# Kernel optimization log

Hardware: AMD Instinct MI355X
Metric: run time of the kernel (lower is better)

## Reference

```python
import jax, jax.numpy as jnp
import numpy as np

N_NODES = 100000
N_EDGES = 1600000
N_GRAPHS = 128
IN_DIM, HID, OUT_DIM, DOC_DIM = 64, 128, 32, 768
LAYERS = 3


def setup_inputs() -> dict:
    key = jax.random.key(0)
    ks = jax.random.split(key, 24)
    s = 0.05
    inp = {
        "x": jax.random.normal(ks[0], (N_NODES, IN_DIM), jnp.float32),
        "doc_features": jax.random.normal(ks[1], (N_GRAPHS, DOC_DIM), jnp.float32),
        "edge_index": jax.random.randint(ks[2], (2, N_EDGES), 0, N_NODES, jnp.int64),
        "batch": jnp.sort(jax.random.randint(ks[3], (N_NODES,), 0, N_GRAPHS, jnp.int64)),
        # parameters (stored as [in, out] so y = x @ W + b)
        "node_w": jax.random.normal(ks[4], (IN_DIM, HID), jnp.float32) * s,
        "node_b": jnp.zeros((HID,), jnp.float32),
        "ggnn_w": jax.random.normal(ks[5], (LAYERS, HID, HID), jnp.float32) * s,
        "gru_w_ih": jax.random.normal(ks[6], (HID, 3 * HID), jnp.float32) * s,
        "gru_b_ih": jnp.zeros((3 * HID,), jnp.float32),
        "gru_w_hh": jax.random.normal(ks[7], (HID, 3 * HID), jnp.float32) * s,
        "gru_b_hh": jnp.zeros((3 * HID,), jnp.float32),
        "doc_w": jax.random.normal(ks[8], (DOC_DIM, HID), jnp.float32) * s,
        "doc_b": jnp.zeros((HID,), jnp.float32),
        "ln_g": jnp.ones((2 * HID,), jnp.float32),
        "ln_b": jnp.zeros((2 * HID,), jnp.float32),
        "fus_w": jax.random.normal(ks[9], (2 * HID, HID), jnp.float32) * s,
        "fus_b": jnp.zeros((HID,), jnp.float32),
        "task_w": jax.random.normal(ks[10], (HID, OUT_DIM), jnp.float32) * s,
        "task_b": jnp.zeros((OUT_DIM,), jnp.float32),
        "time_w": jax.random.normal(ks[11], (HID, 1), jnp.float32) * s,
        "time_b": jnp.zeros((1,), jnp.float32),
    }
    return inp


def _gru(m, h, w_ih, b_ih, w_hh, b_hh):
    gi = m @ w_ih + b_ih  # [N, 3H]
    gh = h @ w_hh + b_hh
    ir, iz, in_ = jnp.split(gi, 3, axis=-1)
    hr, hz, hn = jnp.split(gh, 3, axis=-1)
    r = jax.nn.sigmoid(ir + hr)
    z = jax.nn.sigmoid(iz + hz)
    n = jnp.tanh(in_ + r * hn)
    return (1.0 - z) * n + z * h


def reference(x, doc_features, node_w, node_b, ggnn_w, gru_w_ih, gru_b_ih,
              gru_w_hh, gru_b_hh, doc_w, doc_b, ln_g, ln_b, fus_w, fus_b,
              task_w, task_b, time_w, time_b, edge_index, batch):
    N = x.shape[0]
    src, dst = edge_index[0], edge_index[1]
    # node projection + ReLU
    h = jax.nn.relu(x @ node_w + node_b)  # [N, H]
    # GatedGraphConv: 3 layers of (linear -> scatter-add over edges -> GRU)
    for i in range(LAYERS):
        m = h @ ggnn_w[i]                              # [N, H]
        agg = jax.ops.segment_sum(m[src], dst, num_segments=N)  # scatter-add
        h = _gru(agg, h, gru_w_ih, gru_b_ih, gru_w_hh, gru_b_hh)
    # global mean pool over graphs
    sums = jax.ops.segment_sum(h, batch, num_segments=N_GRAPHS)  # [G, H]
    cnt = jax.ops.segment_sum(jnp.ones((N,), h.dtype), batch, num_segments=N_GRAPHS)
    pooled = sums / jnp.maximum(cnt, 1.0)[:, None]
    # doc projection + fusion head
    doc_emb = jax.nn.relu(doc_features @ doc_w + doc_b)  # [G, H]
    fusion = jnp.concatenate([pooled, doc_emb], axis=1)  # [G, 2H]
    mu = jnp.mean(fusion, axis=-1, keepdims=True)
    var = jnp.mean(jnp.square(fusion - mu), axis=-1, keepdims=True)
    fusion = (fusion - mu) * jax.lax.rsqrt(var + 1e-5) * ln_g + ln_b
    fusion = jax.nn.relu(fusion @ fus_w + fus_b)  # dropout is identity (eval)
    task_output = fusion @ task_w + task_b
    time_output = fusion @ time_w + time_b
    return (task_output, time_output)
```

## Files before the change

### kernel.cpp

```cpp
#include <hip/hip_runtime.h>

#define N_NODES  100000
#define N_EDGES  1600000
#define N_GRAPHS 128
#define SCAN_BLOCKS 98

typedef unsigned short u16;
typedef unsigned int   u32;
typedef __attribute__((ext_vector_type(8))) short short8;
typedef __attribute__((ext_vector_type(4))) float f32x4;

__device__ __forceinline__ float bf2f(u16 v) {
  union { u32 i; float f; } u; u.i = ((u32)v) << 16; return u.f;
}
__device__ __forceinline__ u16 f2bf(float f) {
  union { float f; u32 i; } u; u.f = f;
  u32 r = (u.i + 0x7fffu + ((u.i >> 16) & 1u)) >> 16;
  return (u16)r;
}
__device__ __forceinline__ float sigmoid_f(float x) { return 1.f / (1.f + __expf(-x)); }
__device__ __forceinline__ float tanh_f(float x) {
  x = fminf(15.f, fmaxf(-15.f, x));
  float e = __expf(2.f * x);
  return (e - 1.f) / (e + 1.f);
}
__device__ __forceinline__ int geti(const int* __restrict__ p, int i, int is64) {
  return p[is64 ? (2 * i) : i];
}

__global__ void detect_i64_kernel(const int* __restrict__ ei, const int* __restrict__ batch,
                                  int* __restrict__ flags) {
  int lane = threadIdx.x;
  {
    long long q = (long long)lane * (3200000 / 2 - 1) / 63;
    int pos = (int)(2 * q + 1);
    unsigned long long m = __ballot(ei[pos] != 0);
    if (lane == 0) flags[0] = (m == 0ull) ? 1 : 0;
  }
  {
    long long q = (long long)lane * (100000 / 2 - 1) / 63;
    int pos = (int)(2 * q + 1);
    unsigned long long m = __ballot(batch[pos] != 0);
    if (lane == 0) flags[1] = (m == 0ull) ? 1 : 0;
  }
}

__global__ void hist_kernel(const int* __restrict__ ei, const int* __restrict__ flags,
                            int* __restrict__ counts, u16* __restrict__ rankb) {
  int e = blockIdx.x * 256 + threadIdx.x;
  if (e < N_EDGES) {
    int f = flags[0];
    int d = geti(ei, N_EDGES + e, f);
    int r = atomicAdd(&counts[d], 1);
    rankb[e] = (u16)r;
  }
}

__global__ __launch_bounds__(1024)
void scanA_kernel(const int* __restrict__ counts, int* __restrict__ blocksums) {
  __shared__ int red[16];
  int i = blockIdx.x * 1024 + threadIdx.x;
  int v = (i < N_NODES) ? counts[i] : 0;
  for (int o = 32; o > 0; o >>= 1) v += __shfl_down(v, o, 64);
  int wv = threadIdx.x >> 6, lane = threadIdx.x & 63;
  if (lane == 0) red[wv] = v;
  __syncthreads();
  if (threadIdx.x < 16) {
    int s = red[threadIdx.x];
    for (int o = 8; o > 0; o >>= 1) s += __shfl_down(s, o, 64);
    if (threadIdx.x == 0) blocksums[blockIdx.x] = s;
  }
}

__global__ void scanB_kernel(const int* __restrict__ blocksums, int* __restrict__ blockbase,
                             int* __restrict__ offsets) {
  if (threadIdx.x == 0) {
    int run = 0;
    for (int b = 0; b < SCAN_BLOCKS; ++b) { blockbase[b] = run; run += blocksums[b]; }
    offsets[N_NODES] = run;
  }
}

__global__ __launch_bounds__(1024)
void scanC_kernel(const int* __restrict__ counts, const int* __restrict__ blockbase,
                  int* __restrict__ offsets) {
  __shared__ int buf[1024];
  int t = threadIdx.x;
  int i = blockIdx.x * 1024 + t;
  int v = (i < N_NODES) ? counts[i] : 0;
  buf[t] = v;
  __syncthreads();
  for (int o = 1; o < 1024; o <<= 1) {
    int add = (t >= o) ? buf[t - o] : 0;
    __syncthreads();
    buf[t] += add;
    __syncthreads();
  }
  if (i < N_NODES) offsets[i] = buf[t] - v + blockbase[blockIdx.x];
}

__global__ void scatter_kernel(const int* __restrict__ ei, const int* __restrict__ flags,
                               const int* __restrict__ offsets, const u16* __restrict__ rankb,
                               int* __restrict__ ssrc) {
  int e = blockIdx.x * 256 + threadIdx.x;
  if (e < N_EDGES) {
    int f = flags[0];
    int d = geti(ei, N_EDGES + e, f);
    ssrc[offsets[d] + (int)rankb[e]] = geti(ei, e, f);
  }
}

__global__ void transpose_kernel(const float* __restrict__ in, u16* __restrict__ out, int K, int N) {
  int i = blockIdx.x * 256 + threadIdx.x;
  if (i < K * N) {
    int k = i / N, n = i % N;
    out[n * K + k] = f2bf(in[i]);
  }
}

__global__ void wprime_kernel(const float* __restrict__ ggnn_w, const float* __restrict__ w_ih,
                              float* __restrict__ wp) {
  int i = blockIdx.x * 256 + threadIdx.x;
  if (i >= 3 * 128 * 384) return;
  int l = i / (128 * 384), r = i % (128 * 384), k = r / 384, c = r % 384;
  const float* W = ggnn_w + l * 128 * 128;
  float s = 0.f;
  for (int j = 0; j < 128; ++j) s += W[k * 128 + j] * w_ih[j * 384 + c];
  wp[i] = s;
}

__global__ void build_b2p_kernel(const float* __restrict__ wp, const float* __restrict__ w_hh,
                                 u16* __restrict__ b2p) {
  int g = blockIdx.x * 256 + threadIdx.x;
  if (g >= 8 * 1536 * 8) return;
  int e = g & 7;
  int grp = g >> 3;
  int ci = grp / 1536;
  int idx = grp % 1536;
  int n_lin = idx % 384;
  int ko = idx / 384;
  int k = ci * 32 + ko * 8 + e;
  float v = (k < 128) ? wp[k * 384 + n_lin] : w_hh[(k - 128) * 384 + n_lin];
  b2p[g] = f2bf(v);
}

__global__ __launch_bounds__(256)
void nodeproj_gemm(const float* __restrict__ A, const u16* __restrict__ BT,
                   const float* __restrict__ bias, u16* __restrict__ out, int M)
{
  constexpr int K_DIM = 64, N_DIM = 128, NT = 8, NCHUNK = 2;
  __shared__ u16 B_lds[N_DIM * 40];
  const int tid = threadIdx.x, lane = tid & 63, w = tid >> 6;
  const int strip = blockIdx.x * 64;
  const int ksub = (lane >> 4) * 8;
  union Frag { uint4 u; short8 s; };
  Frag af[NCHUNK];
  const int m_node = strip + w * 16 + (lane & 15);
  const bool avalid = (m_node < M);
#pragma unroll
  for (int ci = 0; ci < NCHUNK; ++ci) {
    int k0 = ci * 32 + ksub;
    short8 sv = {0,0,0,0,0,0,0,0};
    if (avalid) {
      const float* p = A + (size_t)m_node * K_DIM + k0;
      float4 f0 = *(const float4*)p;
      float4 f1 = *(const float4*)(p + 4);
      sv[0]=(short)f2bf(f0.x); sv[1]=(short)f2bf(f0.y); sv[2]=(short)f2bf(f0.z); sv[3]=(short)f2bf(f0.w);
      sv[4]=(short)f2bf(f1.x); sv[5]=(short)f2bf(f1.y); sv[6]=(short)f2bf(f1.z); sv[7]=(short)f2bf(f1.w);
    }
    af[ci].s = sv;
  }
  f32x4 acc[NT];
#pragma unroll
  for (int t = 0; t < NT; ++t) acc[t] = {0.f, 0.f, 0.f, 0.f};
  const int boff = (lane & 15) * 40 + ksub;
#pragma unroll
  for (int ci = 0; ci < NCHUNK; ++ci) {
    if (ci) __syncthreads();
    for (int g = tid; g < N_DIM * 4; g += 256) {
      int n = g >> 2, ko = g & 3;
      uint4 bv = *(const uint4*)(BT + (size_t)n * K_DIM + ci * 32 + ko * 8);
      *(uint4*)(&B_lds[n * 40 + ko * 8]) = bv;
    }
    __syncthreads();
    short8 a = af[ci].s;
#pragma unroll
    for (int t = 0; t < NT; ++t) {
      const short8 b = *(const short8*)(&B_lds[t * 16 * 40 + boff]);
      acc[t] = __builtin_amdgcn_mfma_f32_16x16x32_bf16(a, b, acc[t], 0, 0, 0);
    }
  }
  const int mrow = (lane >> 4) * 4;
#pragma unroll
  for (int t = 0; t < NT; ++t) {
    int col = t * 16 + (lane & 15);
    float bv = bias[col];
#pragma unroll
    for (int r = 0; r < 4; ++r) {
      int node = strip + w * 16 + mrow + r;
      if (node < M) out[(size_t)node * N_DIM + col] = f2bf(fmaxf(acc[t][r] + bv, 0.f));
    }
  }
}

__global__ __launch_bounds__(256)
void gru_gemm(const u16* __restrict__ agg, const u16* __restrict__ h,
              const u16* __restrict__ b2p, const float* __restrict__ b_ih,
              const float* __restrict__ b_hh, u16* __restrict__ hout, int M)
{
  const int tid  = threadIdx.x;
  const int lane = tid & 63;
  const int qc   = tid >> 6;
  const int strip = blockIdx.x * 32;
  const int lrow  = lane & 15;
  const int quad  = lane >> 4;
  const int ksub  = quad * 8;
  if (strip >= M) return;

  f32x4 ar[2][2], az[2][2], ain[2][2], ahn[2][2];
#pragma unroll
  for (int s = 0; s < 2; ++s)
#pragma unroll
    for (int t = 0; t < 2; ++t) {
      ar[s][t] = {0.f,0.f,0.f,0.f}; az[s][t] = {0.f,0.f,0.f,0.f};
      ain[s][t] = {0.f,0.f,0.f,0.f}; ahn[s][t] = {0.f,0.f,0.f,0.f};
    }

  union Frag { uint4 u; short8 s8; };
  const int node0 = strip + lrow;
  const int node1 = strip + 16 + lrow;
  const u16* bb = b2p + ((size_t)quad * 384 + qc * 32 + lrow) * 8;

  Frag a0[2], a1[2], fbr[2][2], fbz[2][2], fbg[2][2];

  auto ldchunk = [&](int ci, int p) {
    const u16* ap = (ci < 4) ? (agg + ci * 32 + ksub) : (h + (ci - 4) * 32 + ksub);
    a0[p].u = *(const uint4*)(ap + (size_t)node0 * 128);
    a1[p].u = *(const uint4*)(ap + (size_t)node1 * 128);
    const u16* cb = bb + ci * 12288;
    fbr[p][0].u = *(const uint4*)(cb);
    fbr[p][1].u = *(const uint4*)(cb + 128);
    fbz[p][0].u = *(const uint4*)(cb + 1024);
    fbz[p][1].u = *(const uint4*)(cb + 1024 + 128);
    fbg[p][0].u = *(const uint4*)(cb + 2048);
    fbg[p][1].u = *(const uint4*)(cb + 2048 + 128);
  };

  ldchunk(0, 0);
#pragma unroll
  for (int ci = 0; ci < 8; ++ci) {
    const int p = ci & 1, q = p ^ 1;
    if (ci < 7) ldchunk(ci + 1, q);
#pragma unroll
    for (int t = 0; t < 2; ++t) {
      ar[0][t] = __builtin_amdgcn_mfma_f32_16x16x32_bf16(a0[p].s8, fbr[p][t].s8, ar[0][t], 0, 0, 0);
      ar[1][t] = __builtin_amdgcn_mfma_f32_16x16x32_bf16(a1[p].s8, fbr[p][t].s8, ar[1][t], 0, 0, 0);
      az[0][t] = __builtin_amdgcn_mfma_f32_16x16x32_bf16(a0[p].s8, fbz[p][t].s8, az[0][t], 0, 0, 0);
      az[1][t] = __builtin_amdgcn_mfma_f32_16x16x32_bf16(a1[p].s8, fbz[p][t].s8, az[1][t], 0, 0, 0);
    }
    if (ci < 4) {
#pragma unroll
      for (int t = 0; t < 2; ++t) {
        ain[0][t] = __builtin_amdgcn_mfma_f32_16x16x32_bf16(a0[p].s8, fbg[p][t].s8, ain[0][t], 0, 0, 0);
        ain[1][t] = __builtin_amdgcn_mfma_f32_16x16x32_bf16(a1[p].s8, fbg[p][t].s8, ain[1][t], 0, 0, 0);
      }
    } else {
#pragma unroll
      for (int t = 0; t < 2; ++t) {
        ahn[0][t] = __builtin_amdgcn_mfma_f32_16x16x32_bf16(a0[p].s8, fbg[p][t].s8, ahn[0][t], 0, 0, 0);
        ahn[1][t] = __builtin_amdgcn_mfma_f32_16x16x32_bf16(a1[p].s8, fbg[p][t].s8, ahn[1][t], 0, 0, 0);
      }
    }
  }

#pragma unroll
  for (int t = 0; t < 2; ++t) {
    const int c = qc * 32 + t * 16 + lrow;
    const float brr = b_ih[c] + b_hh[c];
    const float bzz = b_ih[128 + c] + b_hh[128 + c];
    const float bin = b_ih[256 + c];
    const float bhn = b_hh[256 + c];
#pragma unroll
    for (int s = 0; s < 2; ++s) {
#pragma unroll
      for (int r = 0; r < 4; ++r) {
        const int nrow = strip + s * 16 + quad * 4 + r;
        float rg = sigmoid_f(ar[s][t][r] + brr);
        float zg = sigmoid_f(az[s][t][r] + bzz);
        float hv = ahn[s][t][r] + bhn;
        float ng = tanh_f(ain[s][t][r] + bin + rg * hv);
        float hp = bf2f(h[(size_t)nrow * 128 + c]);
        hout[(size_t)nrow * 128 + c] = f2bf((1.f - zg) * ng + zg * hp);
      }
    }
  }
}

__global__ __launch_bounds__(256)
void agg_kernel(const u16* __restrict__ m, const int* __restrict__ ssrc,
                const int* __restrict__ offsets, u16* __restrict__ agg)
{
  int node = blockIdx.x * 4 + (threadIdx.x >> 6);
  int lane = threadIdx.x & 63;
  if (node >= N_NODES) return;
  const int g = lane >> 4, l = lane & 15;
  int beg = offsets[node], end = offsets[node + 1];
  float s[8] = {0.f,0.f,0.f,0.f,0.f,0.f,0.f,0.f};
  for (int e = beg; e < end; e += 8) {
    uint4 v0 = {0u,0u,0u,0u}, v1 = {0u,0u,0u,0u};
    int e0 = e + g, e1 = e + 4 + g;
    if (e0 < end) { int src = ssrc[e0]; v0 = *(const uint4*)(m + (size_t)src * 128 + l * 8); }
    if (e1 < end) { int src = ssrc[e1]; v1 = *(const uint4*)(m + (size_t)src * 128 + l * 8); }
    u32 w0[4] = {v0.x, v0.y, v0.z, v0.w};
    u32 w1[4] = {v1.x, v1.y, v1.z, v1.w};
#pragma unroll
    for (int i = 0; i < 4; ++i) {
      s[2*i]   += bf2f((u16)(w0[i] & 0xffffu)) + bf2f((u16)(w1[i] & 0xffffu));
      s[2*i+1] += bf2f((u16)(w0[i] >> 16))     + bf2f((u16)(w1[i] >> 16));
    }
  }
#pragma unroll
  for (int i = 0; i < 8; ++i) {
    s[i] += __shfl_xor(s[i], 16, 64);
    s[i] += __shfl_xor(s[i], 32, 64);
  }
  if (g == 0) {
    uint4 o;
    o.x = (u32)f2bf(s[0]) | ((u32)f2bf(s[1]) << 16);
    o.y = (u32)f2bf(s[2]) | ((u32)f2bf(s[3]) << 16);
    o.z = (u32)f2bf(s[4]) | ((u32)f2bf(s[5]) << 16);
    o.w = (u32)f2bf(s[6]) | ((u32)f2bf(s[7]) << 16);
    *(uint4*)(agg + (size_t)node * 128 + l * 8) = o;
  }
}

__global__ __launch_bounds__(256)
void pool_kernel(const u16* __restrict__ h, const int* __restrict__ batch,
                 const int* __restrict__ flags, float* __restrict__ sums)
{
  const int c = threadIdx.x & 127;
  const int half = threadIdx.x >> 7;
  const int base = blockIdx.x * 128;
  const int f = flags[1];
  int gcur = -1; float s = 0.f;
  for (int i = half; i < 128; i += 2) {
    int n = base + i;
    if (n >= N_NODES) break;
    int g = geti(batch, n, f);
    if (g != gcur) {
      if (gcur >= 0) atomicAdd(&sums[gcur * 128 + c], s);
      s = 0.f; gcur = g;
    }
    s += bf2f(h[(size_t)n * 128 + c]);
  }
  if (gcur >= 0) atomicAdd(&sums[gcur * 128 + c], s);
}

__global__ __launch_bounds__(256)
void head2_kernel(const float* __restrict__ sums, const int* __restrict__ batch,
                  const int* __restrict__ flags,
                  const float* __restrict__ doc, const float* __restrict__ doc_w, const float* __restrict__ doc_b,
                  const float* __restrict__ ln_g, const float* __restrict__ ln_b,
                  const float* __restrict__ fus_w, const float* __restrict__ fus_b,
                  const float* __restrict__ task_w, const float* __restrict__ task_b,
                  const float* __restrict__ time_w, const float* __restrict__ time_b,
                  float* __restrict__ out_task, float* __restrict__ out_time)
{
  const int g = blockIdx.x;
  const int t = threadIdx.x;
  __shared__ float fusion[256];
  __shared__ float fh[128];
  __shared__ float dpart[256];
  __shared__ int seg[2];

  if (t < 2) {
    int f = flags[1];
    int target = g + t, lo = 0, hi = N_NODES;
    while (lo < hi) { int mid = (lo + hi) >> 1; if (geti(batch, mid, f) < target) lo = mid + 1; else hi = mid; }
    seg[t] = lo;
  }
  {
    int c = t & 127, kh = t >> 7;
    float s = 0.f;
    for (int k = kh * 384; k < kh * 384 + 384; ++k) s += doc[g * 768 + k] * doc_w[k * 128 + c];
    dpart[t] = s;
  }
  __syncthreads();

  if (t < 128) {
    float cnt = (float)(seg[1] - seg[0]);
    fusion[t] = sums[g * 128 + t] / fmaxf(cnt, 1.f);
  } else {
    int c = t - 128;
    fusion[t] = fmaxf(dpart[c] + dpart[c + 128] + doc_b[c], 0.f);
  }
  __syncthreads();

  float mu = 0.f;
  for (int i = 0; i < 256; ++i) mu += fusion[i];
  mu *= (1.f / 256.f);
  float var = 0.f;
  for (int i = 0; i < 256; ++i) { float d = fusion[i] - mu; var += d * d; }
  var *= (1.f / 256.f);
  float inv = rsqrtf(var + 1e-5f);
  float norm = (fusion[t] - mu) * inv * ln_g[t] + ln_b[t];
  __syncthreads();
  fusion[t] = norm;
  __syncthreads();

  if (t < 128) {
    float s = 0.f;
    for (int k = 0; k < 256; ++k) s += fusion[k] * fus_w[k * 128 + t];
    s += fus_b[t];
    fh[t] = fmaxf(s, 0.f);
  }
  __syncthreads();

  if (t < 32) {
    float s = 0.f;
    for (int k = 0; k < 128; ++k) s += fh[k] * task_w[k * 32 + t];
    s += task_b[t];
    out_task[g * 32 + t] = s;
  }
  if (t == 32) {
    float s = 0.f;
    for (int k = 0; k < 128; ++k) s += fh[k] * time_w[k];
    s += time_b[0];
    out_time[g] = s;
  }
}

extern "C" void kernel_launch(void* const* d_in, const int* in_sizes, int n_in,
                              void* d_out, int out_size, void* d_ws, size_t ws_size,
                              hipStream_t stream)
{
  const float* x        = (const float*)d_in[0];
  const float* doc      = (const float*)d_in[1];
  const int*   ei       = (const int*)d_in[2];
  const int*   batch    = (const int*)d_in[3];
  const float* node_w   = (const float*)d_in[4];
  const float* node_b   = (const float*)d_in[5];
  const float* ggnn_w   = (const float*)d_in[6];
  const float* gru_w_ih = (const float*)d_in[7];
  const float* gru_b_ih = (const float*)d_in[8];
  const float* gru_w_hh = (const float*)d_in[9];
  const float* gru_b_hh = (const float*)d_in[10];
  const float* doc_w    = (const float*)d_in[11];
  const float* doc_b    = (const float*)d_in[12];
  const float* ln_g     = (const float*)d_in[13];
  const float* ln_b     = (const float*)d_in[14];
  const float* fus_w    = (const float*)d_in[15];
  const float* fus_b    = (const float*)d_in[16];
  const float* task_w   = (const float*)d_in[17];
  const float* task_b   = (const float*)d_in[18];
  const float* time_w   = (const float*)d_in[19];
  const float* time_b   = (const float*)d_in[20];

  char* ws = (char*)d_ws;
  size_t off = 0;
  auto alloc = [&](size_t bytes) -> void* {
    void* p = ws + off;
    off = (off + bytes + 255) & ~(size_t)255;
    return p;
  };
  u16* aggb   = (u16*)alloc((size_t)N_NODES * 128 * 2);
  u16* hA     = (u16*)alloc((size_t)N_NODES * 128 * 2);
  u16* hB     = (u16*)alloc((size_t)N_NODES * 128 * 2);
  u16* nwT    = (u16*)alloc(64 * 128 * 2);
  u16* b2p    = (u16*)alloc(3 * 8 * 1536 * 8 * 2);
  float* wp   = (float*)alloc(3 * 128 * 384 * 4);
  float* sums = (float*)alloc(N_GRAPHS * 128 * 4);
  int* counts = (int*)alloc((size_t)N_NODES * 4);
  int* offs   = (int*)alloc((size_t)(N_NODES + 1) * 4);
  int* ssrc   = (int*)alloc((size_t)N_EDGES * 4);
  u16* rankb  = (u16*)alloc((size_t)N_EDGES * 2);
  int* bsum   = (int*)alloc(SCAN_BLOCKS * 4);
  int* bbase  = (int*)alloc(SCAN_BLOCKS * 4);
  int* flags  = (int*)alloc(2 * 4);

  hipMemsetAsync(counts, 0, (size_t)N_NODES * 4, stream);
  hipMemsetAsync(sums, 0, (size_t)N_GRAPHS * 128 * 4, stream);

  detect_i64_kernel<<<1, 64, 0, stream>>>(ei, batch, flags);
  hist_kernel<<<(N_EDGES + 255) / 256, 256, 0, stream>>>(ei, flags, counts, rankb);
  scanA_kernel<<<SCAN_BLOCKS, 1024, 0, stream>>>(counts, bsum);
  scanB_kernel<<<1, 64, 0, stream>>>(bsum, bbase, offs);
  scanC_kernel<<<SCAN_BLOCKS, 1024, 0, stream>>>(counts, bbase, offs);
  scatter_kernel<<<(N_EDGES + 255) / 256, 256, 0, stream>>>(ei, flags, offs, rankb, ssrc);

  transpose_kernel<<<(64 * 128 + 255) / 256, 256, 0, stream>>>(node_w, nwT, 64, 128);
  wprime_kernel<<<(3 * 128 * 384 + 255) / 256, 256, 0, stream>>>(ggnn_w, gru_w_ih, wp);
  for (int l = 0; l < 3; ++l)
    build_b2p_kernel<<<(8 * 1536 * 8 + 255) / 256, 256, 0, stream>>>(
        wp + l * 128 * 384, gru_w_hh, b2p + (size_t)l * 8 * 1536 * 8);

  const int GB = (N_NODES + 63) / 64;
  const int GB32 = N_NODES / 32;
  nodeproj_gemm<<<GB, 256, 0, stream>>>(x, nwT, node_b, hA, N_NODES);

  u16* hcur = hA;
  u16* hnext = hB;
  for (int l = 0; l < 3; ++l) {
    agg_kernel<<<(N_NODES + 3) / 4, 256, 0, stream>>>(hcur, ssrc, offs, aggb);
    gru_gemm<<<GB32, 256, 0, stream>>>(aggb, hcur, b2p + (size_t)l * 8 * 1536 * 8,
                                       gru_b_ih, gru_b_hh, hnext, N_NODES);
    u16* tmp = hcur; hcur = hnext; hnext = tmp;
  }

  pool_kernel<<<(N_NODES + 127) / 128, 256, 0, stream>>>(hcur, batch, flags, sums);

  float* out_task = (float*)d_out;
  float* out_time = out_task + N_GRAPHS * 32;
  head2_kernel<<<N_GRAPHS, 256, 0, stream>>>(sums, batch, flags, doc, doc_w, doc_b, ln_g, ln_b,
                                             fus_w, fus_b, task_w, task_b, time_w, time_b,
                                             out_task, out_time);
}
```

Baseline: 678.2 us.

## Build CSR via two-pass bucketed counting sort with shared-memory atomics

Replaces the global-atomic histogram and random scatter CSR build with a two-level bucket sort. Edges are first binned into 256-node buckets using per-block shared-memory histograms, then counted and placed per node within each bucket in LDS. The goal is to avoid contended global atomics and scattered global writes. It adds several kernel launches and an extra pass over the edges, and it reuses the aggb buffer as scratch space.

After: 634.6 us. 1.07x faster.

```diff
diff --git a/kernel.cpp b/kernel.cpp
--- a/kernel.cpp
+++ b/kernel.cpp
@@ -3,7 +3,15 @@
 #define N_NODES  100000
 #define N_EDGES  1600000
 #define N_GRAPHS 128
-#define SCAN_BLOCKS 98
+
+#define BSH      8
+#define BNODES   (1 << BSH)
+#define NBUCK    391
+#define NBLK_P1  512
+#define EPB      (N_EDGES / NBLK_P1)
+#define BKT_SCAN_N   (NBUCK * NBLK_P1)
+#define SCAN_BLK_BKT 196
+#define SCAN_BLK_NODE 98
 
 typedef unsigned short u16;
 typedef unsigned int   u32;
@@ -45,22 +53,82 @@
   }
 }
 
-__global__ void hist_kernel(const int* __restrict__ ei, const int* __restrict__ flags,
-                            int* __restrict__ counts, u16* __restrict__ rankb) {
-  int e = blockIdx.x * 256 + threadIdx.x;
-  if (e < N_EDGES) {
-    int f = flags[0];
+
+__global__ __launch_bounds__(256)
+void bucket_hist(const int* __restrict__ ei, const int* __restrict__ flags,
+                 int* __restrict__ bcounts) {
+  __shared__ int h[NBUCK];
+  const int f = flags[0];
+  for (int b = threadIdx.x; b < NBUCK; b += 256) h[b] = 0;
+  __syncthreads();
+  const int e0 = blockIdx.x * EPB;
+  for (int i = threadIdx.x; i < EPB; i += 256) {
+    int d = geti(ei, N_EDGES + e0 + i, f);
+    atomicAdd(&h[d >> BSH], 1);
+  }
+  __syncthreads();
+  for (int b = threadIdx.x; b < NBUCK; b += 256)
+    bcounts[b * NBLK_P1 + blockIdx.x] = h[b];
+}
+
+__global__ __launch_bounds__(256)
+void bucket_scatter(const int* __restrict__ ei, const int* __restrict__ flags,
+                    const int* __restrict__ bbases, u32* __restrict__ bedges) {
+  __shared__ int cur[NBUCK];
+  const int f = flags[0];
+  for (int b = threadIdx.x; b < NBUCK; b += 256)
+    cur[b] = bbases[b * NBLK_P1 + blockIdx.x];
+  __syncthreads();
+  const int e0 = blockIdx.x * EPB;
+  for (int i = threadIdx.x; i < EPB; i += 256) {
+    int e = e0 + i;
     int d = geti(ei, N_EDGES + e, f);
-    int r = atomicAdd(&counts[d], 1);
-    rankb[e] = (u16)r;
+    int s = geti(ei, e, f);
+    int pos = atomicAdd(&cur[d >> BSH], 1);
+    bedges[pos] = ((u32)(d & (BNODES - 1)) << 17) | (u32)s;
+  }
+}
+
+__global__ __launch_bounds__(256)
+void node_count(const u32* __restrict__ bedges, const int* __restrict__ bbases,
+                int* __restrict__ counts) {
+  __shared__ int h[BNODES];
+  const int b = blockIdx.x;
+  for (int i = threadIdx.x; i < BNODES; i += 256) h[i] = 0;
+  __syncthreads();
+  const int beg = bbases[b * NBLK_P1];
+  const int end = (b + 1 < NBUCK) ? bbases[(b + 1) * NBLK_P1] : N_EDGES;
+  for (int e = beg + threadIdx.x; e < end; e += 256)
+    atomicAdd(&h[bedges[e] >> 17], 1);
+  __syncthreads();
+  const int node0 = b << BSH;
+  for (int i = threadIdx.x; i < BNODES; i += 256)
+    if (node0 + i < N_NODES) counts[node0 + i] = h[i];
+}
+
+__global__ __launch_bounds__(256)
+void final_scatter(const u32* __restrict__ bedges, const int* __restrict__ bbases,
+                   const int* __restrict__ offs, int* __restrict__ ssrc) {
+  __shared__ int cur[BNODES];
+  const int b = blockIdx.x;
+  const int node0 = b << BSH;
+  for (int i = threadIdx.x; i < BNODES; i += 256)
+    cur[i] = (node0 + i < N_NODES) ? offs[node0 + i] : 0;
+  __syncthreads();
+  const int beg = bbases[b * NBLK_P1];
+  const int end = (b + 1 < NBUCK) ? bbases[(b + 1) * NBLK_P1] : N_EDGES;
+  for (int e = beg + threadIdx.x; e < end; e += 256) {
+    u32 v = bedges[e];
+    int pos = atomicAdd(&cur[v >> 17], 1);
+    ssrc[pos] = (int)(v & 0x1FFFFu);
   }
 }
 
 __global__ __launch_bounds__(1024)
-void scanA_kernel(const int* __restrict__ counts, int* __restrict__ blocksums) {
+void scanA_kernel(const int* __restrict__ counts, int n, int* __restrict__ blocksums) {
   __shared__ int red[16];
   int i = blockIdx.x * 1024 + threadIdx.x;
-  int v = (i < N_NODES) ? counts[i] : 0;
+  int v = (i < n) ? counts[i] : 0;
   for (int o = 32; o > 0; o >>= 1) v += __shfl_down(v, o, 64);
   int wv = threadIdx.x >> 6, lane = threadIdx.x & 63;
   if (lane == 0) red[wv] = v;
@@ -72,22 +140,22 @@
   }
 }
 
-__global__ void scanB_kernel(const int* __restrict__ blocksums, int* __restrict__ blockbase,
-                             int* __restrict__ offsets) {
+__global__ void scanB_kernel(const int* __restrict__ blocksums, int nblocks,
+                             int* __restrict__ blockbase, int* __restrict__ total_out) {
   if (threadIdx.x == 0) {
     int run = 0;
-    for (int b = 0; b < SCAN_BLOCKS; ++b) { blockbase[b] = run; run += blocksums[b]; }
-    offsets[N_NODES] = run;
+    for (int b = 0; b < nblocks; ++b) { blockbase[b] = run; run += blocksums[b]; }
+    if (total_out) *total_out = run;
   }
 }
 
 __global__ __launch_bounds__(1024)
-void scanC_kernel(const int* __restrict__ counts, const int* __restrict__ blockbase,
+void scanC_kernel(const int* __restrict__ counts, int n, const int* __restrict__ blockbase,
                   int* __restrict__ offsets) {
   __shared__ int buf[1024];
   int t = threadIdx.x;
   int i = blockIdx.x * 1024 + t;
-  int v = (i < N_NODES) ? counts[i] : 0;
+  int v = (i < n) ? counts[i] : 0;
   buf[t] = v;
   __syncthreads();
   for (int o = 1; o < 1024; o <<= 1) {
@@ -96,18 +164,7 @@
     buf[t] += add;
     __syncthreads();
   }
-  if (i < N_NODES) offsets[i] = buf[t] - v + blockbase[blockIdx.x];
-}
-
-__global__ void scatter_kernel(const int* __restrict__ ei, const int* __restrict__ flags,
-                               const int* __restrict__ offsets, const u16* __restrict__ rankb,
-                               int* __restrict__ ssrc) {
-  int e = blockIdx.x * 256 + threadIdx.x;
-  if (e < N_EDGES) {
-    int f = flags[0];
-    int d = geti(ei, N_EDGES + e, f);
-    ssrc[offsets[d] + (int)rankb[e]] = geti(ei, e, f);
-  }
+  if (i < n) offsets[i] = buf[t] - v + blockbase[blockIdx.x];
 }
 
 __global__ void transpose_kernel(const float* __restrict__ in, u16* __restrict__ out, int K, int N) {
@@ -463,30 +520,38 @@
     off = (off + bytes + 255) & ~(size_t)255;
     return p;
   };
-  u16* aggb   = (u16*)alloc((size_t)N_NODES * 128 * 2);
-  u16* hA     = (u16*)alloc((size_t)N_NODES * 128 * 2);
-  u16* hB     = (u16*)alloc((size_t)N_NODES * 128 * 2);
-  u16* nwT    = (u16*)alloc(64 * 128 * 2);
-  u16* b2p    = (u16*)alloc(3 * 8 * 1536 * 8 * 2);
-  float* wp   = (float*)alloc(3 * 128 * 384 * 4);
-  float* sums = (float*)alloc(N_GRAPHS * 128 * 4);
-  int* counts = (int*)alloc((size_t)N_NODES * 4);
-  int* offs   = (int*)alloc((size_t)(N_NODES + 1) * 4);
-  int* ssrc   = (int*)alloc((size_t)N_EDGES * 4);
-  u16* rankb  = (u16*)alloc((size_t)N_EDGES * 2);
-  int* bsum   = (int*)alloc(SCAN_BLOCKS * 4);
-  int* bbase  = (int*)alloc(SCAN_BLOCKS * 4);
-  int* flags  = (int*)alloc(2 * 4);
-
-  hipMemsetAsync(counts, 0, (size_t)N_NODES * 4, stream);
+  u16* aggb    = (u16*)alloc((size_t)N_NODES * 128 * 2);
+  u16* hA      = (u16*)alloc((size_t)N_NODES * 128 * 2);
+  u16* hB      = (u16*)alloc((size_t)N_NODES * 128 * 2);
+  u16* nwT     = (u16*)alloc(64 * 128 * 2);
+  u16* b2p     = (u16*)alloc(3 * 8 * 1536 * 8 * 2);
+  float* wp    = (float*)alloc(3 * 128 * 384 * 4);
+  float* sums  = (float*)alloc(N_GRAPHS * 128 * 4);
+  int* counts  = (int*)alloc((size_t)N_NODES * 4);
+  int* offs    = (int*)alloc((size_t)(N_NODES + 1) * 4);
+  int* ssrc    = (int*)alloc((size_t)N_EDGES * 4);
+  int* bsum    = (int*)alloc(SCAN_BLK_BKT * 4);
+  int* bbase   = (int*)alloc(SCAN_BLK_BKT * 4);
+  int* flags   = (int*)alloc(2 * 4);
+
+  u32* bedges  = (u32*)aggb;
+  int* bcounts = (int*)((char*)aggb + 6400000);
+  int* bbases  = (int*)((char*)aggb + 7200768);
+
   hipMemsetAsync(sums, 0, (size_t)N_GRAPHS * 128 * 4, stream);
 
   detect_i64_kernel<<<1, 64, 0, stream>>>(ei, batch, flags);
-  hist_kernel<<<(N_EDGES + 255) / 256, 256, 0, stream>>>(ei, flags, counts, rankb);
-  scanA_kernel<<<SCAN_BLOCKS, 1024, 0, stream>>>(counts, bsum);
-  scanB_kernel<<<1, 64, 0, stream>>>(bsum, bbase, offs);
-  scanC_kernel<<<SCAN_BLOCKS, 1024, 0, stream>>>(counts, bbase, offs);
-  scatter_kernel<<<(N_EDGES + 255) / 256, 256, 0, stream>>>(ei, flags, offs, rankb, ssrc);
+
+  bucket_hist<<<NBLK_P1, 256, 0, stream>>>(ei, flags, bcounts);
+  scanA_kernel<<<SCAN_BLK_BKT, 1024, 0, stream>>>(bcounts, BKT_SCAN_N, bsum);
+  scanB_kernel<<<1, 64, 0, stream>>>(bsum, SCAN_BLK_BKT, bbase, (int*)nullptr);
+  scanC_kernel<<<SCAN_BLK_BKT, 1024, 0, stream>>>(bcounts, BKT_SCAN_N, bbase, bbases);
+  bucket_scatter<<<NBLK_P1, 256, 0, stream>>>(ei, flags, bbases, bedges);
+  node_count<<<NBUCK, 256, 0, stream>>>(bedges, bbases, counts);
+  scanA_kernel<<<SCAN_BLK_NODE, 1024, 0, stream>>>(counts, N_NODES, bsum);
+  scanB_kernel<<<1, 64, 0, stream>>>(bsum, SCAN_BLK_NODE, bbase, offs + N_NODES);
+  scanC_kernel<<<SCAN_BLK_NODE, 1024, 0, stream>>>(counts, N_NODES, bbase, offs);
+  final_scatter<<<NBUCK, 256, 0, stream>>>(bedges, bbases, offs, ssrc);
 
   transpose_kernel<<<(64 * 128 + 255) / 256, 256, 0, stream>>>(node_w, nwT, 64, 128);
   wprime_kernel<<<(3 * 128 * 384 + 255) / 256, 256, 0, stream>>>(ggnn_w, gru_w_ih, wp);
```
